# Kernel optimization log

Measured on AMD Instinct MI355X. Metric: run time of the kernel, lower is better.

## Reference

```python
import jax, jax.numpy as jnp
import numpy as np

B, T, D, H = 4, 2048, 1024, 16
DK, DV, CHUNK = D // H, 2 * D // H, 64  # head_k_dim=64, head_v_dim=128 (expand_v=2.0)
EPS = 1e-5


def setup_inputs() -> dict:
    key = jax.random.key(0)
    ks = jax.random.split(key, 6)
    s = 0.02
    return {
        "x": jax.random.normal(ks[0], (B, T, D), jnp.float32),
        "Wq": jax.random.normal(ks[1], (D, H * DK), jnp.float32) * s,
        "Wk": jax.random.normal(ks[2], (D, H * DK), jnp.float32) * s,
        "Wv": jax.random.normal(ks[3], (D, H * DV), jnp.float32) * s,
        "Wg": jax.random.normal(ks[4], (D, H * DV), jnp.float32) * s,
        "Wo": jax.random.normal(ks[5], (H * DV, D), jnp.float32) * s,
        "g_norm_w": jnp.ones((DV,), jnp.float32),
    }


def _rope(q):
    # q: [B, T, H, DK]; non-interleaved (rotate-half) rotary, base 10000
    half = DK // 2
    inv_freq = 1.0 / (10000.0 ** (jnp.arange(half, dtype=jnp.float32) / half))
    freqs = jnp.arange(T, dtype=jnp.float32)[:, None] * inv_freq  # [T, half]
    cos = jnp.cos(freqs)[None, :, None, :]
    sin = jnp.sin(freqs)[None, :, None, :]
    q1, q2 = q[..., :half], q[..., half:]
    return jnp.concatenate([q1 * cos - q2 * sin, q2 * cos + q1 * sin], axis=-1)


def reference(x, Wq, Wk, Wv, Wg, Wo, g_norm_w):
    q = _rope((x @ Wq).reshape(B, T, H, DK)) * (DK ** -0.5)
    k = _rope((x @ Wk).reshape(B, T, H, DK))
    v = (x @ Wv).reshape(B, T, H, DV)

    N = T // CHUNK
    def tochunks(t):  # [B,T,H,Dh] -> [N,B,H,C,Dh]
        return t.reshape(B, N, CHUNK, H, t.shape[-1]).transpose(1, 0, 3, 2, 4)
    qc, kc, vc = tochunks(q), tochunks(k), tochunks(v)

    # per-head RetNet decay: gamma_h = 1 - 2^{-5-h}
    gamma = 1.0 - jnp.exp2(-5.0 - jnp.arange(H, dtype=jnp.float32))  # [H]
    i = jnp.arange(CHUNK, dtype=jnp.float32)
    # intra-chunk decay mask D[h,i,j] = gamma^{i-j} for j<=i else 0
    Dmask = jnp.where(i[:, None] >= i[None, :],
                      gamma[:, None, None] ** (i[:, None] - i[None, :]), 0.0)  # [H,C,C]
    cross = gamma[:, None] ** (i + 1.0)          # [H,C] query decay vs prev state
    kdec = gamma[:, None] ** (CHUNK - 1.0 - i)   # [H,C] key decay into new state
    chunk_dec = gamma ** CHUNK                   # [H]

    def step(S, qkv):
        q_, k_, v_ = qkv  # [B,H,C,DK], [B,H,C,DK], [B,H,C,DV]
        attn = jnp.einsum('bhid,bhjd->bhij', q_, k_) * Dmask
        o = jnp.einsum('bhij,bhjv->bhiv', attn, v_)
        o = o + jnp.einsum('bhid,bhdv->bhiv', q_ * cross[None, :, :, None], S)
        S = S * chunk_dec[None, :, None, None] + \
            jnp.einsum('bhjd,bhjv->bhdv', k_ * kdec[None, :, :, None], v_)
        return S, o

    S0 = jnp.zeros((B, H, DK, DV), x.dtype)
    _, o = jax.lax.scan(step, S0, (qc, kc, vc))  # [N,B,H,C,DV]
    o = o.transpose(1, 0, 3, 2, 4).reshape(B, T, H, DV)

    # fused RMSNorm + swish gate (FusedRMSNormSwishGate)
    g = (x @ Wg).reshape(B, T, H, DV)
    o = o * jax.lax.rsqrt(jnp.mean(o * o, axis=-1, keepdims=True) + EPS) * g_norm_w
    o = o * (g * jax.nn.sigmoid(g))
    return o.reshape(B, T, H * DV) @ Wo
```

## Files before the change

### kernel.cpp

```cpp
#include <hip/hip_runtime.h>
#include <hip/hip_bf16.h>
#include <math.h>

typedef unsigned short u16;
typedef unsigned int u32;
typedef __attribute__((ext_vector_type(8))) short bf16x8;
typedef __attribute__((ext_vector_type(4))) float f32x4;


__device__ __forceinline__ u16 f2bf(float f) {
  union { float f; unsigned u; } a; a.f = f;
  unsigned u = a.u;
  unsigned r = (u + 0x7fffu + ((u >> 16) & 1u)) >> 16;
  return (u16)r;
}
__device__ __forceinline__ float bf2f(u16 s) {
  union { unsigned u; float f; } a; a.u = ((unsigned)s) << 16; return a.f;
}

__global__ void k_sentinel(float* out) {
  if (threadIdx.x == 0 && blockIdx.x == 0) out[0] = 1.0e6f;
}

__device__ __forceinline__ void split8r(const float* t, bf16x8& hi, bf16x8& lo) {
#pragma unroll
  for (int m = 0; m < 8; ++m) {
    union { float f; u32 u; } c; c.f = t[m];
    union { u32 u; float f; } hf; hf.u = c.u & 0xffff0000u;
    union { float f; u32 u; } lw; lw.f = t[m] - hf.f;
    hi[m] = (short)(u16)(c.u >> 16);
    lo[m] = (short)(u16)(lw.u >> 16);
  }
}
__device__ __forceinline__ void split8p(const float* __restrict__ p, bf16x8& hi, bf16x8& lo) {
  f32x4 a = *(const f32x4*)p;
  f32x4 b = *(const f32x4*)(p + 4);
  float t[8];
  t[0]=a[0]; t[1]=a[1]; t[2]=a[2]; t[3]=a[3]; t[4]=b[0]; t[5]=b[1]; t[6]=b[2]; t[7]=b[3];
  split8r(t, hi, lo);
}

__device__ __forceinline__ void bar_lds() {
  asm volatile("s_waitcnt lgkmcnt(0)" ::: "memory");
  __builtin_amdgcn_sched_barrier(0);
  __builtin_amdgcn_s_barrier();
}

__device__ __forceinline__ void gload16(const u16* g, u16* l) {
  __builtin_amdgcn_global_load_lds(
      (const __attribute__((address_space(1))) unsigned int*)g,
      (__attribute__((address_space(3))) unsigned int*)l, 16, 0, 0);
}

__global__ __launch_bounds__(256) void k_cvt_x(const float* __restrict__ src, u16* __restrict__ dst) {
  int i = blockIdx.x * 256 + threadIdx.x;
  float4 v = ((const float4*)src)[i];
  ushort4 o;
  o.x = f2bf(v.x); o.y = f2bf(v.y); o.z = f2bf(v.z); o.w = f2bf(v.w);
  ((ushort4*)dst)[i] = o;
}

__global__ __launch_bounds__(256) void k_ropetab(float2* __restrict__ tab) {
  int idx = blockIdx.x * 256 + threadIdx.x;
  int t = idx >> 5, i = idx & 31;
  float invf = powf(10000.f, -(float)i * (1.f / 32.f));
  float ang = (float)t * invf;
  float2 cs; cs.x = cosf(ang); cs.y = sinf(ang);
  tab[idx] = cs;
}

__global__ __launch_bounds__(256) void k_transpose_all(
    const float* __restrict__ Wq, const float* __restrict__ Wk, const float* __restrict__ Wv,
    const float* __restrict__ Wg, const float* __restrict__ Wo,
    u16* __restrict__ Wqkb, u16* __restrict__ Wvgb, u16* __restrict__ Wob) {
  int z = blockIdx.x;
  const float* src; u16* dst; int K, N, bx, by;
  if (z < 1024)      { src = Wq; dst = Wqkb;                       K = 1024; N = 1024; int r = z;        bx = r & 31; by = r >> 5; }
  else if (z < 2048) { src = Wk; dst = Wqkb + (size_t)1024 * 1024; K = 1024; N = 1024; int r = z - 1024; bx = r & 31; by = r >> 5; }
  else if (z < 4096) { src = Wv; dst = Wvgb;                       K = 1024; N = 2048; int r = z - 2048; bx = r & 63; by = r >> 6; }
  else if (z < 6144) { src = Wg; dst = Wvgb + (size_t)2048 * 1024; K = 1024; N = 2048; int r = z - 4096; bx = r & 63; by = r >> 6; }
  else               { src = Wo; dst = Wob;                        K = 2048; N = 1024; int r = z - 6144; bx = r & 31; by = r >> 5; }
  __shared__ float tile[32][33];
  int n0 = bx * 32, k0 = by * 32;
  int tx = threadIdx.x & 31, ty = threadIdx.x >> 5;
  for (int r = 0; r < 32; r += 8)
    tile[ty + r][tx] = src[(size_t)(k0 + ty + r) * N + n0 + tx];
  __syncthreads();
  for (int r = 0; r < 32; r += 8)
    dst[(size_t)(n0 + ty + r) * K + k0 + tx] = f2bf(tile[tx][ty + r]);
}

__global__ __launch_bounds__(256, 2) void k_gemm_qkvg(const u16* __restrict__ A, const u16* __restrict__ Bt,
                                                      float* __restrict__ qk, u16* __restrict__ vg,
                                                      const float2* __restrict__ tab, int K) {
  __shared__ __attribute__((aligned(16))) u16 As[128 * 32];
  __shared__ __attribute__((aligned(16))) u16 Bs[128 * 32];
  int nbx = gridDim.x;
  int id = blockIdx.y * nbx + blockIdx.x;
  int cpx = (nbx * gridDim.y) >> 3;
  int sw = (id & 7) * cpx + (id >> 3);
  int bx = sw % nbx, by = sw / nbx;
  int i0 = by * 128, n0 = bx * 128;
  int tid = threadIdx.x;
  int lane = tid & 63, w = tid >> 6;
  int wr = (w >> 1) * 64, wc = (w & 1) * 64;
  int srow = lane >> 2, scol = (lane & 3) * 8;
  f32x4 acc[4][4];
#pragma unroll
  for (int m = 0; m < 4; ++m)
#pragma unroll
    for (int n = 0; n < 4; ++n) acc[m][n] = (f32x4){0.f, 0.f, 0.f, 0.f};
  int fr = lane & 15, kb = (lane >> 4) * 8;
  for (int k0 = 0; k0 < K; k0 += 32) {
    __syncthreads();
#pragma unroll
    for (int q = 0; q < 2; ++q) {
      int s = w * 2 + q;
      gload16(&A[(size_t)(i0 + s * 16 + srow) * K + k0 + scol], &As[s * 512]);
      gload16(&Bt[(size_t)(n0 + s * 16 + srow) * K + k0 + scol], &Bs[s * 512]);
    }
    asm volatile("s_waitcnt vmcnt(0)" ::: "memory");
    __syncthreads();
    bf16x8 af[4], bfr[4];
#pragma unroll
    for (int m = 0; m < 4; ++m) af[m] = *(const bf16x8*)&As[(wr + m * 16 + fr) * 32 + kb];
#pragma unroll
    for (int n = 0; n < 4; ++n) bfr[n] = *(const bf16x8*)&Bs[(wc + n * 16 + fr) * 32 + kb];
#pragma unroll
    for (int m = 0; m < 4; ++m)
#pragma unroll
      for (int n = 0; n < 4; ++n)
        acc[m][n] = __builtin_amdgcn_mfma_f32_16x16x32_bf16(af[m], bfr[n], acc[m][n], 0, 0, 0);
  }
  int rb = (lane >> 4) * 4, cb = lane & 15;
  if (n0 < 2048) {
    float scale = (n0 < 1024) ? 0.125f : 1.0f;
#pragma unroll
    for (int m = 0; m < 4; ++m)
#pragma unroll
      for (int n = 0; n < 2; ++n) {
        int gc = n0 + wc + n * 16 + cb;
        int ii = n * 16 + cb;
#pragma unroll
        for (int r = 0; r < 4; ++r) {
          int gr = i0 + wr + m * 16 + rb + r;
          int t = gr & 2047;
          float2 cs = tab[t * 32 + ii];
          float q1 = acc[m][n][r], q2 = acc[m][n + 2][r];
          qk[(size_t)gr * 2048 + gc]      = (q1 * cs.x - q2 * cs.y) * scale;
          qk[(size_t)gr * 2048 + gc + 32] = (q2 * cs.x + q1 * cs.y) * scale;
        }
      }
  } else {
#pragma unroll
    for (int m = 0; m < 4; ++m)
#pragma unroll
      for (int n = 0; n < 4; ++n) {
        int gr = i0 + wr + m * 16 + rb;
        int gc = n0 - 2048 + wc + n * 16 + cb;
#pragma unroll
        for (int r = 0; r < 4; ++r)
          vg[(size_t)(gr + r) * 4096 + gc] = f2bf(acc[m][n][r]);
      }
  }
}

__global__ __launch_bounds__(256, 2) void k_gemm_out(const u16* __restrict__ A, const u16* __restrict__ Bt,
                                                     float* __restrict__ Cv, int N, int K) {
  __shared__ __attribute__((aligned(16))) u16 As[128 * 32];
  __shared__ __attribute__((aligned(16))) u16 Bs[128 * 32];
  int nbx = gridDim.x;
  int id = blockIdx.y * nbx + blockIdx.x;
  int cpx = (nbx * gridDim.y) >> 3;
  int sw = (id & 7) * cpx + (id >> 3);
  int bx = sw % nbx, by = sw / nbx;
  int i0 = by * 128, n0 = bx * 128;
  int tid = threadIdx.x;
  int lane = tid & 63, w = tid >> 6;
  int wr = (w >> 1) * 64, wc = (w & 1) * 64;
  int srow = lane >> 2, scol = (lane & 3) * 8;
  f32x4 acc[4][4];
#pragma unroll
  for (int m = 0; m < 4; ++m)
#pragma unroll
    for (int n = 0; n < 4; ++n) acc[m][n] = (f32x4){0.f, 0.f, 0.f, 0.f};
  int fr = lane & 15, kb = (lane >> 4) * 8;
  for (int k0 = 0; k0 < K; k0 += 32) {
    __syncthreads();
#pragma unroll
    for (int q = 0; q < 2; ++q) {
      int s = w * 2 + q;
      gload16(&A[(size_t)(i0 + s * 16 + srow) * K + k0 + scol], &As[s * 512]);
      gload16(&Bt[(size_t)(n0 + s * 16 + srow) * K + k0 + scol], &Bs[s * 512]);
    }
    asm volatile("s_waitcnt vmcnt(0)" ::: "memory");
    __syncthreads();
    bf16x8 af[4], bfr[4];
#pragma unroll
    for (int m = 0; m < 4; ++m) af[m] = *(const bf16x8*)&As[(wr + m * 16 + fr) * 32 + kb];
#pragma unroll
    for (int n = 0; n < 4; ++n) bfr[n] = *(const bf16x8*)&Bs[(wc + n * 16 + fr) * 32 + kb];
#pragma unroll
    for (int m = 0; m < 4; ++m)
#pragma unroll
      for (int n = 0; n < 4; ++n)
        acc[m][n] = __builtin_amdgcn_mfma_f32_16x16x32_bf16(af[m], bfr[n], acc[m][n], 0, 0, 0);
  }
  int rb = (lane >> 4) * 4, cb = lane & 15;
#pragma unroll
  for (int m = 0; m < 4; ++m)
#pragma unroll
    for (int n = 0; n < 4; ++n) {
      int gr = i0 + wr + m * 16 + rb;
      int gc = n0 + wc + n * 16 + cb;
#pragma unroll
      for (int r = 0; r < 4; ++r)
        Cv[(size_t)(gr + r) * N + gc] = acc[m][n][r];
    }
}

__global__ __launch_bounds__(512) void k_retention(const float* __restrict__ qk, const u16* __restrict__ vg,
                                                   const float* __restrict__ gnw, u16* __restrict__ og) {
  int bh = blockIdx.x & 63, rq = blockIdx.x >> 6;
  int h = bh & 15, b = bh >> 4;
  int gi0 = rq * 16;

  __shared__ __attribute__((aligned(16))) float qs[16][68];
  __shared__ __attribute__((aligned(16))) float ks[64][68];
  __shared__ __attribute__((aligned(16))) u16 vst[128][88];
  __shared__ __attribute__((aligned(16))) u16 kta_h[8][520];
  __shared__ __attribute__((aligned(16))) u16 kta_l[8][520];
  __shared__ __attribute__((aligned(16))) u16 pa_h[16][68];
  __shared__ __attribute__((aligned(16))) u16 pa_l[16][68];
  __shared__ __attribute__((aligned(16))) u16 sst_h[8][1040];
  __shared__ __attribute__((aligned(16))) u16 sst_l[8][1040];
  __shared__ float dpow[72];
  __shared__ float ssred[8][16];

  int tid = threadIdx.x;
  int w = tid >> 6, l = tid & 63;
  int fr = l & 15, fq = l >> 4;
  float gamma = 1.f - exp2f(-5.f - (float)h);
  if (tid <= 64) dpow[tid] = powf(gamma, (float)tid);
  for (int c = tid; c < 4160; c += 512) { ((u32*)sst_h)[c] = 0; ((u32*)sst_l)[c] = 0; }
  __syncthreads();
  float cdec = dpow[64];

  int e0 = w * 16;
  float gww = gnw[e0 + fr];
  int khmax = (rq < 2) ? 1 : 2;

  int qi = tid >> 4, qd4 = (tid & 15) * 4;
  int sj = tid >> 3, sdg = (tid & 7) * 8;
  int vjp = tid & 31, ve8 = (tid >> 5) * 8;

  f32x4 Sacc[4][2];
#pragma unroll
  for (int dt = 0; dt < 4; ++dt)
#pragma unroll
    for (int nt = 0; nt < 2; ++nt) Sacc[dt][nt] = (f32x4){0.f, 0.f, 0.f, 0.f};

  f32x4 pq = (f32x4){0.f, 0.f, 0.f, 0.f};
  f32x4 pk0, pk1;
  bf16x8 pva, pvb;
  {
    int rowbase = b * 2048;
    if (tid < 256) pq = *(const f32x4*)&qk[(size_t)(rowbase + gi0 + qi) * 2048 + h * 64 + qd4];
    const float* kr = &qk[(size_t)(rowbase + sj) * 2048 + 1024 + h * 64 + sdg];
    pk0 = *(const f32x4*)kr;
    pk1 = *(const f32x4*)(kr + 4);
    const u16* vr = &vg[(size_t)(rowbase + 2 * vjp) * 4096 + h * 128 + ve8];
    pva = *(const bf16x8*)vr;
    pvb = *(const bf16x8*)(vr + 4096);
  }

  for (int n = 0; n < 32; ++n) {
    int rowbase = b * 2048 + n * 64;
    if (tid < 256) *(f32x4*)&qs[qi][qd4] = pq;
    {
      *(f32x4*)&ks[sj][sdg] = pk0;
      *(f32x4*)&ks[sj][sdg + 4] = pk1;
      float kdv = dpow[63 - sj];
      float kd[8];
#pragma unroll
      for (int m = 0; m < 4; ++m) { kd[m] = pk0[m] * kdv; kd[m + 4] = pk1[m] * kdv; }
      bf16x8 kh8, kl8;
      split8r(kd, kh8, kl8);
      int J = sj >> 3, s = sj & 7, dh = tid & 7;
#pragma unroll
      for (int m = 0; m < 8; ++m) {
        int blk = (dh * 8) | (m ^ dh);
        kta_h[J][blk * 8 + s] = (u16)kh8[m];
        kta_l[J][blk * 8 + s] = (u16)kl8[m];
      }
#pragma unroll
      for (int m = 0; m < 8; ++m)
        *(u32*)&vst[ve8 + m][2 * vjp] = (u32)(u16)pva[m] | ((u32)(u16)pvb[m] << 16);
    }
    __syncthreads();
    if (n < 31) {
      int rb2 = rowbase + 64;
      if (tid < 256) pq = *(const f32x4*)&qk[(size_t)(rb2 + gi0 + qi) * 2048 + h * 64 + qd4];
      const float* kr = &qk[(size_t)(rb2 + sj) * 2048 + 1024 + h * 64 + sdg];
      pk0 = *(const f32x4*)kr;
      pk1 = *(const f32x4*)(kr + 4);
      const u16* vr = &vg[(size_t)(rb2 + 2 * vjp) * 4096 + h * 128 + ve8];
      pva = *(const bf16x8*)vr;
      pvb = *(const bf16x8*)(vr + 4096);
    }
    bf16x8 qhc[2], qlc[2];
    split8p(&qs[fr][fq * 8], qhc[0], qlc[0]);
    split8p(&qs[fr][32 + fq * 8], qhc[1], qlc[1]);
    if (w < 4) {
      int ct = w;
      f32x4 at = (f32x4){0.f, 0.f, 0.f, 0.f};
      if (16 * ct <= gi0 + 15) {
#pragma unroll
        for (int kh = 0; kh < 2; ++kh) {
          bf16x8 kbh, kbl;
          split8p(&ks[16 * ct + fr][kh * 32 + fq * 8], kbh, kbl);
          at = __builtin_amdgcn_mfma_f32_16x16x32_bf16(kbh, qhc[kh], at, 0, 0, 0);
          at = __builtin_amdgcn_mfma_f32_16x16x32_bf16(kbl, qhc[kh], at, 0, 0, 0);
          at = __builtin_amdgcn_mfma_f32_16x16x32_bf16(kbh, qlc[kh], at, 0, 0, 0);
        }
      }
      int jb = 16 * ct + fq * 4;
      ushort4 wh, wl;
#pragma unroll
      for (int r = 0; r < 4; ++r) {
        int s = gi0 + fr - (jb + r);
        float val = (s >= 0) ? at[r] * dpow[s] : 0.f;
        union { float f; u32 u; } c; c.f = val;
        union { u32 u; float f; } hf; hf.u = c.u & 0xffff0000u;
        union { float f; u32 u; } lw; lw.f = val - hf.f;
        ((u16*)&wh)[r] = (u16)(c.u >> 16);
        ((u16*)&wl)[r] = (u16)(lw.u >> 16);
      }
      *(ushort4*)&pa_h[fr][jb] = wh;
      *(ushort4*)&pa_l[fr][jb] = wl;
    } else if (n < 31) {
      int eb = (w - 4) * 32;
#pragma unroll
      for (int dt = 0; dt < 4; ++dt)
#pragma unroll
        for (int nt = 0; nt < 2; ++nt)
#pragma unroll
          for (int r = 0; r < 4; ++r) Sacc[dt][nt][r] *= cdec;
      bf16x8 bv[2][2];
#pragma unroll
      for (int kh2 = 0; kh2 < 2; ++kh2)
#pragma unroll
        for (int nt = 0; nt < 2; ++nt)
          bv[kh2][nt] = *(const bf16x8*)&vst[eb + nt * 16 + fr][kh2 * 32 + fq * 8];
#pragma unroll
      for (int kh2 = 0; kh2 < 2; ++kh2) {
#pragma unroll
        for (int dt = 0; dt < 4; ++dt) {
          int d = dt * 16 + fr;
          int blk = d ^ ((dt * 2 + (fr >> 3)) & 7);
          bf16x8 ah = *(const bf16x8*)&kta_h[kh2 * 4 + fq][blk * 8];
          bf16x8 al = *(const bf16x8*)&kta_l[kh2 * 4 + fq][blk * 8];
#pragma unroll
          for (int nt = 0; nt < 2; ++nt) {
            Sacc[dt][nt] = __builtin_amdgcn_mfma_f32_16x16x32_bf16(ah, bv[kh2][nt], Sacc[dt][nt], 0, 0, 0);
            Sacc[dt][nt] = __builtin_amdgcn_mfma_f32_16x16x32_bf16(al, bv[kh2][nt], Sacc[dt][nt], 0, 0, 0);
          }
        }
      }
    }
    bar_lds();
    f32x4 o1 = (f32x4){0.f, 0.f, 0.f, 0.f};
    f32x4 o2 = (f32x4){0.f, 0.f, 0.f, 0.f};
#pragma unroll
    for (int kh2 = 0; kh2 < 2; ++kh2) {
      bf16x8 sh = *(const bf16x8*)&sst_h[kh2 * 4 + fq][(e0 + fr) * 8];
      bf16x8 sl = *(const bf16x8*)&sst_l[kh2 * 4 + fq][(e0 + fr) * 8];
      o2 = __builtin_amdgcn_mfma_f32_16x16x32_bf16(qhc[kh2], sh, o2, 0, 0, 0);
      o2 = __builtin_amdgcn_mfma_f32_16x16x32_bf16(qhc[kh2], sl, o2, 0, 0, 0);
      o2 = __builtin_amdgcn_mfma_f32_16x16x32_bf16(qlc[kh2], sh, o2, 0, 0, 0);
      if (kh2 < khmax) {
        bf16x8 ph = *(const bf16x8*)&pa_h[fr][kh2 * 32 + fq * 8];
        bf16x8 pl = *(const bf16x8*)&pa_l[fr][kh2 * 32 + fq * 8];
        bf16x8 bvv = *(const bf16x8*)&vst[e0 + fr][kh2 * 32 + fq * 8];
        o1 = __builtin_amdgcn_mfma_f32_16x16x32_bf16(ph, bvv, o1, 0, 0, 0);
        o1 = __builtin_amdgcn_mfma_f32_16x16x32_bf16(pl, bvv, o1, 0, 0, 0);
      }
    }
    float ofin[4], ssp[4];
#pragma unroll
    for (int r = 0; r < 4; ++r) {
      int gi = gi0 + fq * 4 + r;
      ofin[r] = o1[r] + dpow[gi + 1] * o2[r];
      ssp[r] = ofin[r] * ofin[r];
    }
#pragma unroll
    for (int r = 0; r < 4; ++r) {
      ssp[r] += __shfl_xor(ssp[r], 1, 64);
      ssp[r] += __shfl_xor(ssp[r], 2, 64);
      ssp[r] += __shfl_xor(ssp[r], 4, 64);
      ssp[r] += __shfl_xor(ssp[r], 8, 64);
    }
    if (fr == 0) {
#pragma unroll
      for (int r = 0; r < 4; ++r) ssred[w][fq * 4 + r] = ssp[r];
    }
    bar_lds();
#pragma unroll
    for (int r = 0; r < 4; ++r) {
      int i16 = fq * 4 + r;
      float tot = 0.f;
#pragma unroll
      for (int w2 = 0; w2 < 8; ++w2) tot += ssred[w2][i16];
      float rms = rsqrtf(tot * (1.f / 128.f) + 1e-5f);
      int grow = rowbase + gi0 + i16;
      float g = bf2f(vg[(size_t)grow * 4096 + 2048 + h * 128 + e0 + fr]);
      float y = ofin[r] * rms * gww * (g / (1.f + expf(-g)));
      og[(size_t)grow * 2048 + h * 128 + e0 + fr] = f2bf(y);
    }
    if (w >= 4 && n < 31) {
      int eb = (w - 4) * 32;
#pragma unroll
      for (int dt = 0; dt < 4; ++dt) {
        int g = dt * 2 + (fq >> 1);
#pragma unroll
        for (int nt = 0; nt < 2; ++nt) {
          int e = eb + nt * 16 + fr;
          ushort4 wh, wl;
#pragma unroll
          for (int r = 0; r < 4; ++r) {
            union { float f; u32 u; } c; c.f = Sacc[dt][nt][r];
            union { u32 u; float f; } hf; hf.u = c.u & 0xffff0000u;
            union { float f; u32 u; } lw; lw.f = Sacc[dt][nt][r] - hf.f;
            ((u16*)&wh)[r] = (u16)(c.u >> 16);
            ((u16*)&wl)[r] = (u16)(lw.u >> 16);
          }
          int idx = e * 8 + (fq & 1) * 4;
          *(ushort4*)&sst_h[g][idx] = wh;
          *(ushort4*)&sst_l[g][idx] = wl;
        }
      }
    }
  }
}

extern "C" void kernel_launch(void* const* d_in, const int* in_sizes, int n_in,
                              void* d_out, int out_size, void* d_ws, size_t ws_size,
                              hipStream_t stream) {
  const float* x   = (const float*)d_in[0];
  const float* Wq  = (const float*)d_in[1];
  const float* Wk  = (const float*)d_in[2];
  const float* Wv  = (const float*)d_in[3];
  const float* Wg  = (const float*)d_in[4];
  const float* Wo  = (const float*)d_in[5];
  const float* gnw = (const float*)d_in[6];
  float* out = (float*)d_out;

  const size_t MB = 1024 * 1024;
  char* ws = (char*)d_ws;
  u16*   xb   = (u16*)(ws + 0 * MB);
  u16*   Wqkb = (u16*)(ws + 16 * MB);
  u16*   Wvgb = (u16*)(ws + 20 * MB);
  float2* tab = (float2*)(ws + 28 * MB);
  float* qk   = (float*)(ws + 32 * MB);
  u16*   vg   = (u16*)(ws + 96 * MB);
  u16*   Wob  = (u16*)(ws + 160 * MB);
  u16*   og   = (u16*)(ws + 0 * MB);
  const size_t NEED = 164 * MB;
  if (ws_size < NEED) {
    k_sentinel<<<1, 64, 0, stream>>>(out);
    return;
  }

  k_cvt_x<<<8192, 256, 0, stream>>>(x, xb);
  k_ropetab<<<256, 256, 0, stream>>>(tab);
  k_transpose_all<<<8192, 256, 0, stream>>>(Wq, Wk, Wv, Wg, Wo, Wqkb, Wvgb, Wob);

  k_gemm_qkvg<<<dim3(48, 64), 256, 0, stream>>>(xb, Wqkb, qk, vg, tab, 1024);
  k_retention<<<256, 512, 0, stream>>>(qk, vg, gnw, og);
  k_gemm_out<<<dim3(8, 64), 256, 0, stream>>>(og, Wob, out, 1024, 2048);
}
```

Measured before the change: 305.0 us.

## Double-buffer LDS tiles in both GEMMs and remap qkvg block swizzle

Both bf16 GEMM kernels now use two LDS buffers, so the global-to-LDS load of the next K tile is issued before the MFMAs on the current tile, with a single barrier per iteration. Wave priority is raised around the MFMA block. The QKVG GEMM also gets a hard-coded grid-to-tile mapping (48 columns, groups of 6x8) meant to improve L2 reuse. The cost is double the LDS per block, which may limit occupancy, and the new mapping assumes a fixed grid shape.

```diff
diff --git a/kernel.cpp b/kernel.cpp
--- a/kernel.cpp
+++ b/kernel.cpp
@@ -42,6 +42,12 @@
 
 __device__ __forceinline__ void bar_lds() {
   asm volatile("s_waitcnt lgkmcnt(0)" ::: "memory");
+  __builtin_amdgcn_sched_barrier(0);
+  __builtin_amdgcn_s_barrier();
+}
+
+__device__ __forceinline__ void bar_vm() {
+  asm volatile("s_waitcnt vmcnt(0)" ::: "memory");
   __builtin_amdgcn_sched_barrier(0);
   __builtin_amdgcn_s_barrier();
 }
@@ -93,8 +99,95 @@
 __global__ __launch_bounds__(256, 2) void k_gemm_qkvg(const u16* __restrict__ A, const u16* __restrict__ Bt,
                                                       float* __restrict__ qk, u16* __restrict__ vg,
                                                       const float2* __restrict__ tab, int K) {
-  __shared__ __attribute__((aligned(16))) u16 As[128 * 32];
-  __shared__ __attribute__((aligned(16))) u16 Bs[128 * 32];
+  __shared__ __attribute__((aligned(16))) u16 As[2][128 * 32];
+  __shared__ __attribute__((aligned(16))) u16 Bs[2][128 * 32];
+  int id = blockIdx.y * 48 + blockIdx.x;
+  int x = id & 7, loc = id >> 3;
+  int bxg = loc / 48, rem = loc - bxg * 48;
+  int by8 = rem / 6, bxi = rem - by8 * 6;
+  int bx = bxg * 6 + bxi, by = x * 8 + by8;
+  int i0 = by * 128, n0 = bx * 128;
+  int tid = threadIdx.x;
+  int lane = tid & 63, w = tid >> 6;
+  int wr = (w >> 1) * 64, wc = (w & 1) * 64;
+  int srow = lane >> 2, scol = (lane & 3) * 8;
+  f32x4 acc[4][4];
+#pragma unroll
+  for (int m = 0; m < 4; ++m)
+#pragma unroll
+    for (int n = 0; n < 4; ++n) acc[m][n] = (f32x4){0.f, 0.f, 0.f, 0.f};
+  int fr = lane & 15, kb = (lane >> 4) * 8;
+  int nkt = K >> 5;
+
+#define STG(t, sl)                                                                   \
+  {                                                                                  \
+    _Pragma("unroll")                                                                \
+    for (int q = 0; q < 2; ++q) {                                                    \
+      int s = w * 2 + q;                                                             \
+      gload16(&A[(size_t)(i0 + s * 16 + srow) * K + (t) * 32 + scol], &As[sl][s * 512]); \
+      gload16(&Bt[(size_t)(n0 + s * 16 + srow) * K + (t) * 32 + scol], &Bs[sl][s * 512]); \
+    }                                                                                \
+  }
+
+  STG(0, 0);
+  bar_vm();
+  int cur = 0;
+  for (int t = 0; t < nkt; ++t) {
+    if (t + 1 < nkt) STG(t + 1, cur ^ 1);
+    bf16x8 af[4], bfr[4];
+#pragma unroll
+    for (int m = 0; m < 4; ++m) af[m] = *(const bf16x8*)&As[cur][(wr + m * 16 + fr) * 32 + kb];
+#pragma unroll
+    for (int n = 0; n < 4; ++n) bfr[n] = *(const bf16x8*)&Bs[cur][(wc + n * 16 + fr) * 32 + kb];
+    __builtin_amdgcn_s_setprio(1);
+#pragma unroll
+    for (int m = 0; m < 4; ++m)
+#pragma unroll
+      for (int n = 0; n < 4; ++n)
+        acc[m][n] = __builtin_amdgcn_mfma_f32_16x16x32_bf16(af[m], bfr[n], acc[m][n], 0, 0, 0);
+    __builtin_amdgcn_s_setprio(0);
+    bar_vm();
+    cur ^= 1;
+  }
+#undef STG
+
+  int rb = (lane >> 4) * 4, cb = lane & 15;
+  if (n0 < 2048) {
+    float scale = (n0 < 1024) ? 0.125f : 1.0f;
+#pragma unroll
+    for (int m = 0; m < 4; ++m)
+#pragma unroll
+      for (int n = 0; n < 2; ++n) {
+        int gc = n0 + wc + n * 16 + cb;
+        int ii = n * 16 + cb;
+#pragma unroll
+        for (int r = 0; r < 4; ++r) {
+          int gr = i0 + wr + m * 16 + rb + r;
+          int t = gr & 2047;
+          float2 cs = tab[t * 32 + ii];
+          float q1 = acc[m][n][r], q2 = acc[m][n + 2][r];
+          qk[(size_t)gr * 2048 + gc]      = (q1 * cs.x - q2 * cs.y) * scale;
+          qk[(size_t)gr * 2048 + gc + 32] = (q2 * cs.x + q1 * cs.y) * scale;
+        }
+      }
+  } else {
+#pragma unroll
+    for (int m = 0; m < 4; ++m)
+#pragma unroll
+      for (int n = 0; n < 4; ++n) {
+        int gr = i0 + wr + m * 16 + rb;
+        int gc = n0 - 2048 + wc + n * 16 + cb;
+#pragma unroll
+        for (int r = 0; r < 4; ++r)
+          vg[(size_t)(gr + r) * 4096 + gc] = f2bf(acc[m][n][r]);
+      }
+  }
+}
+
+__global__ __launch_bounds__(256, 2) void k_gemm_out(const u16* __restrict__ A, const u16* __restrict__ Bt,
+                                                     float* __restrict__ Cv, int N, int K) {
+  __shared__ __attribute__((aligned(16))) u16 As[2][128 * 32];
+  __shared__ __attribute__((aligned(16))) u16 Bs[2][128 * 32];
   int nbx = gridDim.x;
   int id = blockIdx.y * nbx + blockIdx.x;
   int cpx = (nbx * gridDim.y) >> 3;
@@ -111,101 +204,40 @@
 #pragma unroll
     for (int n = 0; n < 4; ++n) acc[m][n] = (f32x4){0.f, 0.f, 0.f, 0.f};
   int fr = lane & 15, kb = (lane >> 4) * 8;
-  for (int k0 = 0; k0 < K; k0 += 32) {
-    __syncthreads();
-#pragma unroll
-    for (int q = 0; q < 2; ++q) {
-      int s = w * 2 + q;
-      gload16(&A[(size_t)(i0 + s * 16 + srow) * K + k0 + scol], &As[s * 512]);
-      gload16(&Bt[(size_t)(n0 + s * 16 + srow) * K + k0 + scol], &Bs[s * 512]);
-    }
-    asm volatile("s_waitcnt vmcnt(0)" ::: "memory");
-    __syncthreads();
+  int nkt = K >> 5;
+
+#define STG(t, sl)                                                                   \
+  {                                                                                  \
+    _Pragma("unroll")                                                                \
+    for (int q = 0; q < 2; ++q) {                                                    \
+      int s = w * 2 + q;                                                             \
+      gload16(&A[(size_t)(i0 + s * 16 + srow) * K + (t) * 32 + scol], &As[sl][s * 512]); \
+      gload16(&Bt[(size_t)(n0 + s * 16 + srow) * K + (t) * 32 + scol], &Bs[sl][s * 512]); \
+    }                                                                                \
+  }
+
+  STG(0, 0);
+  bar_vm();
+  int cur = 0;
+  for (int t = 0; t < nkt; ++t) {
+    if (t + 1 < nkt) STG(t + 1, cur ^ 1);
     bf16x8 af[4], bfr[4];
 #pragma unroll
-    for (int m = 0; m < 4; ++m) af[m] = *(const bf16x8*)&As[(wr + m * 16 + fr) * 32 + kb];
-#pragma unroll
-    for (int n = 0; n < 4; ++n) bfr[n] = *(const bf16x8*)&Bs[(wc + n * 16 + fr) * 32 + kb];
+    for (int m = 0; m < 4; ++m) af[m] = *(const bf16x8*)&As[cur][(wr + m * 16 + fr) * 32 + kb];
+#pragma unroll
+    for (int n = 0; n < 4; ++n) bfr[n] = *(const bf16x8*)&Bs[cur][(wc + n * 16 + fr) * 32 + kb];
+    __builtin_amdgcn_s_setprio(1);
 #pragma unroll
     for (int m = 0; m < 4; ++m)
 #pragma unroll
       for (int n = 0; n < 4; ++n)
         acc[m][n] = __builtin_amdgcn_mfma_f32_16x16x32_bf16(af[m], bfr[n], acc[m][n], 0, 0, 0);
-  }
-  int rb = (lane >> 4) * 4, cb = lane & 15;
-  if (n0 < 2048) {
-    float scale = (n0 < 1024) ? 0.125f : 1.0f;
-#pragma unroll
-    for (int m = 0; m < 4; ++m)
-#pragma unroll
-      for (int n = 0; n < 2; ++n) {
-        int gc = n0 + wc + n * 16 + cb;
-        int ii = n * 16 + cb;
-#pragma unroll
-        for (int r = 0; r < 4; ++r) {
-          int gr = i0 + wr + m * 16 + rb + r;
-          int t = gr & 2047;
-          float2 cs = tab[t * 32 + ii];
-          float q1 = acc[m][n][r], q2 = acc[m][n + 2][r];
-          qk[(size_t)gr * 2048 + gc]      = (q1 * cs.x - q2 * cs.y) * scale;
-          qk[(size_t)gr * 2048 + gc + 32] = (q2 * cs.x + q1 * cs.y) * scale;
-        }
-      }
-  } else {
-#pragma unroll
-    for (int m = 0; m < 4; ++m)
-#pragma unroll
-      for (int n = 0; n < 4; ++n) {
-        int gr = i0 + wr + m * 16 + rb;
-        int gc = n0 - 2048 + wc + n * 16 + cb;
-#pragma unroll
-        for (int r = 0; r < 4; ++r)
-          vg[(size_t)(gr + r) * 4096 + gc] = f2bf(acc[m][n][r]);
-      }
-  }
-}
-
-__global__ __launch_bounds__(256, 2) void k_gemm_out(const u16* __restrict__ A, const u16* __restrict__ Bt,
-                                                     float* __restrict__ Cv, int N, int K) {
-  __shared__ __attribute__((aligned(16))) u16 As[128 * 32];
-  __shared__ __attribute__((aligned(16))) u16 Bs[128 * 32];
-  int nbx = gridDim.x;
-  int id = blockIdx.y * nbx + blockIdx.x;
-  int cpx = (nbx * gridDim.y) >> 3;
-  int sw = (id & 7) * cpx + (id >> 3);
-  int bx = sw % nbx, by = sw / nbx;
-  int i0 = by * 128, n0 = bx * 128;
-  int tid = threadIdx.x;
-  int lane = tid & 63, w = tid >> 6;
-  int wr = (w >> 1) * 64, wc = (w & 1) * 64;
-  int srow = lane >> 2, scol = (lane & 3) * 8;
-  f32x4 acc[4][4];
-#pragma unroll
-  for (int m = 0; m < 4; ++m)
-#pragma unroll
-    for (int n = 0; n < 4; ++n) acc[m][n] = (f32x4){0.f, 0.f, 0.f, 0.f};
-  int fr = lane & 15, kb = (lane >> 4) * 8;
-  for (int k0 = 0; k0 < K; k0 += 32) {
-    __syncthreads();
-#pragma unroll
-    for (int q = 0; q < 2; ++q) {
-      int s = w * 2 + q;
-      gload16(&A[(size_t)(i0 + s * 16 + srow) * K + k0 + scol], &As[s * 512]);
-      gload16(&Bt[(size_t)(n0 + s * 16 + srow) * K + k0 + scol], &Bs[s * 512]);
-    }
-    asm volatile("s_waitcnt vmcnt(0)" ::: "memory");
-    __syncthreads();
-    bf16x8 af[4], bfr[4];
-#pragma unroll
-    for (int m = 0; m < 4; ++m) af[m] = *(const bf16x8*)&As[(wr + m * 16 + fr) * 32 + kb];
-#pragma unroll
-    for (int n = 0; n < 4; ++n) bfr[n] = *(const bf16x8*)&Bs[(wc + n * 16 + fr) * 32 + kb];
-#pragma unroll
-    for (int m = 0; m < 4; ++m)
-#pragma unroll
-      for (int n = 0; n < 4; ++n)
-        acc[m][n] = __builtin_amdgcn_mfma_f32_16x16x32_bf16(af[m], bfr[n], acc[m][n], 0, 0, 0);
-  }
+    __builtin_amdgcn_s_setprio(0);
+    bar_vm();
+    cur ^= 1;
+  }
+#undef STG
+
   int rb = (lane >> 4) * 4, cb = lane & 15;
 #pragma unroll
   for (int m = 0; m < 4; ++m)
```

Result: no change. 301.5 us (-1.2%).
